# Kernel optimization log

Hardware: AMD Instinct MI355X
Metric: run time of the kernel (lower is better)

Reference implementation:

```python
import jax, jax.numpy as jnp
import numpy as np

S, B, D, H, F, E = 2048, 2, 768, 12, 3072, 8
DH = D // H
T = S * B
CAP = int(2.0 * T / E)  # capacity factor 2.0


def layer_norm(x, g, b, eps=1e-5):
    m = jnp.mean(x, axis=-1, keepdims=True)
    v = jnp.var(x, axis=-1, keepdims=True)
    return (x - m) * jax.lax.rsqrt(v + eps) * g + b


def setup_inputs() -> dict:
    key = jax.random.key(0)
    ks = jax.random.split(key, 16)
    sc = 0.02
    return {
        "src": jax.random.normal(ks[0], (S, B, D), jnp.float32),
        "in_proj_w": sc * jax.random.normal(ks[1], (3 * D, D), jnp.float32),
        "in_proj_b": sc * jax.random.normal(ks[2], (3 * D,), jnp.float32),
        "out_proj_w": sc * jax.random.normal(ks[3], (D, D), jnp.float32),
        "out_proj_b": sc * jax.random.normal(ks[4], (D,), jnp.float32),
        "norm1_g": 1.0 + sc * jax.random.normal(ks[5], (D,), jnp.float32),
        "norm1_b": sc * jax.random.normal(ks[6], (D,), jnp.float32),
        "router_w": sc * jax.random.normal(ks[7], (E, D), jnp.float32),
        "router_b": sc * jax.random.normal(ks[8], (E,), jnp.float32),
        "w1": sc * jax.random.normal(ks[9], (E, D, F), jnp.float32),
        "b1": sc * jax.random.normal(ks[10], (E, F), jnp.float32),
        "w2": sc * jax.random.normal(ks[11], (E, F, D), jnp.float32),
        "b2": sc * jax.random.normal(ks[12], (E, D), jnp.float32),
        "norm2_g": 1.0 + sc * jax.random.normal(ks[13], (D,), jnp.float32),
        "norm2_b": sc * jax.random.normal(ks[14], (D,), jnp.float32),
    }


def reference(src, in_proj_w, in_proj_b, out_proj_w, out_proj_b,
              norm1_g, norm1_b, router_w, router_b, w1, b1, w2, b2,
              norm2_g, norm2_b):
    # ---- multi-head self-attention (dropout = identity, eval mode) ----
    qkv = src @ in_proj_w.T + in_proj_b                # [S,B,3D]
    q, k, v = jnp.split(qkv, 3, axis=-1)

    def heads(t):  # [S,B,D] -> [B,H,S,DH]
        return t.reshape(S, B, H, DH).transpose(1, 2, 0, 3)

    q, k, v = heads(q), heads(k), heads(v)
    scores = jnp.einsum('bhsd,bhtd->bhst', q, k) / np.float32(np.sqrt(DH))
    attn = jax.nn.softmax(scores, axis=-1)
    ctx = jnp.einsum('bhst,bhtd->bhsd', attn, v)       # [B,H,S,DH]
    ctx = ctx.transpose(2, 0, 1, 3).reshape(S, B, D)
    attn_out = ctx @ out_proj_w.T + out_proj_b

    x = layer_norm(src + attn_out, norm1_g, norm1_b)

    # ---- Switch MoE FFN: top-1 routing, capacity-based dispatch ----
    tok = x.reshape(T, D)
    logits = tok @ router_w.T + router_b               # [T,E]
    probs = jax.nn.softmax(logits, axis=-1)
    eidx = jnp.argmax(probs, axis=-1)                  # [T]
    gate = jnp.take_along_axis(probs, eidx[:, None], axis=-1)[:, 0]
    oh = jax.nn.one_hot(eidx, E, dtype=probs.dtype)    # [T,E]
    # position of each token within its expert's queue
    pos = (jnp.cumsum(oh, axis=0) * oh).sum(-1).astype(jnp.int32) - 1

    # scatter tokens into per-expert buffers (tokens over capacity dropped)
    buf = jnp.zeros((E, CAP, D), tok.dtype).at[eidx, pos].set(tok, mode='drop')
    h = jax.nn.relu(jnp.einsum('ecd,edf->ecf', buf, w1) + b1[:, None, :])
    y = jnp.einsum('ecf,efd->ecd', h, w2) + b2[:, None, :]

    keep = pos < CAP
    out_tok = jnp.where(keep[:, None], y[eidx, jnp.minimum(pos, CAP - 1)], 0.0)
    out_tok = out_tok * gate[:, None]
    moe_out = out_tok.reshape(S, B, D)

    # load-balancing loss: E * sum_e(frac_tokens_e * mean_prob_e)
    f = oh.mean(axis=0)
    P = probs.mean(axis=0)
    lb_loss = E * jnp.sum(f * P)

    out = layer_norm(x + moe_out, norm2_g, norm2_b)
    return (out, lb_loss)
```

## Files before the change

kernel.cpp:

```cpp
#include <hip/hip_runtime.h>
#include <hip/hip_bf16.h>


#define S_   2048
#define B_   2
#define D_   768
#define H_   12
#define DH_  64
#define F_   3072
#define E_   8
#define T_   4096
#define CAP_ 1024

#define AP_  68

typedef __hip_bfloat16 bf16;
using short8  = __attribute__((ext_vector_type(8))) short;
using floatx4 = __attribute__((ext_vector_type(4))) float;

__device__ __forceinline__ float b2f(bf16 x) { return __bfloat162float(x); }
__device__ __forceinline__ bf16  f2b(float x) { return __float2bfloat16(x); }

struct SrcPair { const bf16* h; const bf16* l; };

__global__ __launch_bounds__(256) void split_kernel(
    const float* __restrict__ x, bf16* __restrict__ h, bf16* __restrict__ l,
    int n4) {
  int i = blockIdx.x * 256 + threadIdx.x;
  if (i >= n4) return;
  float4 v = ((const float4*)x)[i];
  float va[4] = {v.x, v.y, v.z, v.w};
  __attribute__((aligned(8))) bf16 hh[4], ll[4];
#pragma unroll
  for (int j = 0; j < 4; j++) {
    bf16 t = f2b(va[j]);
    hh[j] = t;
    ll[j] = f2b(va[j] - b2f(t));
  }
  *(uint2*)(h + (size_t)i * 4) = *(const uint2*)hh;
  *(uint2*)(l + (size_t)i * 4) = *(const uint2*)ll;
}

__device__ __forceinline__ void gemm_split_loop(
    SrcPair A, SrcPair W, int K,
    bf16* AsH, bf16* AsL, bf16* WsH, bf16* WsL, floatx4 (&acc)[4][4]) {
  const int tid = threadIdx.x;
  const int w = tid >> 6, lane = tid & 63;
  const int srow = lane >> 2;
  const int scol = (lane & 3) * 8;
  const int r0 = w * 32 + srow;
  const int lds0 = (w * 32 + srow) * 32 + scol;
  const int wm = (w >> 1) * 64, wn = (w & 1) * 64;
  const int fr = lane & 15, g = lane >> 4;

  size_t o0 = (size_t)r0 * K + scol;
  size_t o1 = (size_t)(r0 + 16) * K + scol;
  short8 ah0 = *(const short8*)(A.h + o0), al0 = *(const short8*)(A.l + o0);
  short8 ah1 = *(const short8*)(A.h + o1), al1 = *(const short8*)(A.l + o1);
  short8 wh0 = *(const short8*)(W.h + o0), wl0 = *(const short8*)(W.l + o0);
  short8 wh1 = *(const short8*)(W.h + o1), wl1 = *(const short8*)(W.l + o1);

  for (int kt = 0; kt < K; kt += 32) {
    o0 += 32; o1 += 32;
    __syncthreads();
    *(short8*)(AsH + lds0)       = ah0;
    *(short8*)(AsH + lds0 + 512) = ah1;
    *(short8*)(AsL + lds0)       = al0;
    *(short8*)(AsL + lds0 + 512) = al1;
    *(short8*)(WsH + lds0)       = wh0;
    *(short8*)(WsH + lds0 + 512) = wh1;
    *(short8*)(WsL + lds0)       = wl0;
    *(short8*)(WsL + lds0 + 512) = wl1;
    __syncthreads();
    if (kt + 32 < K) {
      ah0 = *(const short8*)(A.h + o0); al0 = *(const short8*)(A.l + o0);
      ah1 = *(const short8*)(A.h + o1); al1 = *(const short8*)(A.l + o1);
      wh0 = *(const short8*)(W.h + o0); wl0 = *(const short8*)(W.l + o0);
      wh1 = *(const short8*)(W.h + o1); wl1 = *(const short8*)(W.l + o1);
    }
    short8 afh[4], afl[4], bfh[4], bfl[4];
#pragma unroll
    for (int mi = 0; mi < 4; mi++) {
      int o = (wm + mi * 16 + fr) * 32 + g * 8;
      afh[mi] = *(const short8*)&AsH[o];
      afl[mi] = *(const short8*)&AsL[o];
    }
#pragma unroll
    for (int ni = 0; ni < 4; ni++) {
      int o = (wn + ni * 16 + fr) * 32 + g * 8;
      bfh[ni] = *(const short8*)&WsH[o];
      bfl[ni] = *(const short8*)&WsL[o];
    }
#pragma unroll
    for (int mi = 0; mi < 4; mi++)
#pragma unroll
      for (int ni = 0; ni < 4; ni++) {
        floatx4 z = acc[mi][ni];
        z = __builtin_amdgcn_mfma_f32_16x16x32_bf16(afh[mi], bfh[ni], z, 0, 0, 0);
        z = __builtin_amdgcn_mfma_f32_16x16x32_bf16(afh[mi], bfl[ni], z, 0, 0, 0);
        z = __builtin_amdgcn_mfma_f32_16x16x32_bf16(afl[mi], bfh[ni], z, 0, 0, 0);
        acc[mi][ni] = z;
      }
  }
}

__global__ __launch_bounds__(256) void gemm_split_pairout(
    SrcPair A, SrcPair W, const float* __restrict__ bias,
    bf16* __restrict__ Chi, bf16* __restrict__ Clo, int N, int K) {
  __shared__ __attribute__((aligned(16))) bf16 AsH[4096], AsL[4096];
  __shared__ __attribute__((aligned(16))) bf16 WsH[4096], WsL[4096];
  const int m0 = blockIdx.y * 128, n0 = blockIdx.x * 128;
  floatx4 acc[4][4];
#pragma unroll
  for (int i = 0; i < 4; i++)
#pragma unroll
    for (int j = 0; j < 4; j++) acc[i][j] = (floatx4){0.f, 0.f, 0.f, 0.f};
  SrcPair Aoff{A.h + (size_t)m0 * K, A.l + (size_t)m0 * K};
  SrcPair Woff{W.h + (size_t)n0 * K, W.l + (size_t)n0 * K};
  gemm_split_loop(Aoff, Woff, K, AsH, AsL, WsH, WsL, acc);

  const int tid = threadIdx.x, w = tid >> 6, lane = tid & 63;
  const int wm = (w >> 1) * 64, wn = (w & 1) * 64;
  const int fr = lane & 15, rg = (lane >> 4) * 4;
#pragma unroll
  for (int mi = 0; mi < 4; mi++) {
#pragma unroll
    for (int ni = 0; ni < 4; ni++) {
      int n = n0 + wn + ni * 16 + fr;
      float bv = bias[n];
#pragma unroll
      for (int r = 0; r < 4; r++) {
        int m = m0 + wm + mi * 16 + rg + r;
        float v = acc[mi][ni][r] + bv;
        bf16 hh = f2b(v);
        Chi[(size_t)m * N + n] = hh;
        Clo[(size_t)m * N + n] = f2b(v - b2f(hh));
      }
    }
  }
}

__global__ __launch_bounds__(256) void gemm_split_f32out(
    SrcPair A, SrcPair W, const float* __restrict__ bias,
    const float* __restrict__ resid, float* __restrict__ C, int N, int K) {
  __shared__ __attribute__((aligned(16))) bf16 AsH[4096], AsL[4096];
  __shared__ __attribute__((aligned(16))) bf16 WsH[4096], WsL[4096];
  const int m0 = blockIdx.y * 128, n0 = blockIdx.x * 128;
  floatx4 acc[4][4];
#pragma unroll
  for (int i = 0; i < 4; i++)
#pragma unroll
    for (int j = 0; j < 4; j++) acc[i][j] = (floatx4){0.f, 0.f, 0.f, 0.f};
  SrcPair Aoff{A.h + (size_t)m0 * K, A.l + (size_t)m0 * K};
  SrcPair Woff{W.h + (size_t)n0 * K, W.l + (size_t)n0 * K};
  gemm_split_loop(Aoff, Woff, K, AsH, AsL, WsH, WsL, acc);

  const int tid = threadIdx.x, w = tid >> 6, lane = tid & 63;
  const int wm = (w >> 1) * 64, wn = (w & 1) * 64;
  const int fr = lane & 15, rg = (lane >> 4) * 4;
#pragma unroll
  for (int mi = 0; mi < 4; mi++) {
#pragma unroll
    for (int ni = 0; ni < 4; ni++) {
      int n = n0 + wn + ni * 16 + fr;
      float bv = bias[n];
#pragma unroll
      for (int r = 0; r < 4; r++) {
        int m = m0 + wm + mi * 16 + rg + r;
        C[(size_t)m * N + n] = acc[mi][ni][r] + bv + resid[(size_t)m * N + n];
      }
    }
  }
}

__device__ __forceinline__ void gemm_tile_loop(
    const bf16* __restrict__ Ablk, const bf16* __restrict__ Wblk, int K,
    bf16* As, bf16* Ws, floatx4 (&acc)[4][4]) {
  const int tid = threadIdx.x;
  const int w = tid >> 6, lane = tid & 63;
  const int srow = lane >> 2;
  const int scol = (lane & 3) * 8;
  const bf16* Ag = Ablk + (size_t)(w * 32 + srow) * K + scol;
  const bf16* Wg = Wblk + (size_t)(w * 32 + srow) * K + scol;
  bf16* AsW = As + (w * 32 + srow) * 32 + scol;
  bf16* WsW = Ws + (w * 32 + srow) * 32 + scol;
  const int wm = (w >> 1) * 64, wn = (w & 1) * 64;
  const int fr = lane & 15, g = lane >> 4;

  short8 a0 = *(const short8*)(Ag);
  short8 a1 = *(const short8*)(Ag + 16 * (size_t)K);
  short8 w0 = *(const short8*)(Wg);
  short8 w1v = *(const short8*)(Wg + 16 * (size_t)K);

  for (int kt = 0; kt < K; kt += 32) {
    Ag += 32; Wg += 32;
    __syncthreads();
    *(short8*)(AsW)           = a0;
    *(short8*)(AsW + 16 * 32) = a1;
    *(short8*)(WsW)           = w0;
    *(short8*)(WsW + 16 * 32) = w1v;
    __syncthreads();
    if (kt + 32 < K) {
      a0 = *(const short8*)(Ag);
      a1 = *(const short8*)(Ag + 16 * (size_t)K);
      w0 = *(const short8*)(Wg);
      w1v = *(const short8*)(Wg + 16 * (size_t)K);
    }
    short8 af[4], bfg[4];
#pragma unroll
    for (int mi = 0; mi < 4; mi++)
      af[mi] = *(const short8*)&As[(wm + mi * 16 + fr) * 32 + g * 8];
#pragma unroll
    for (int ni = 0; ni < 4; ni++)
      bfg[ni] = *(const short8*)&Ws[(wn + ni * 16 + fr) * 32 + g * 8];
#pragma unroll
    for (int mi = 0; mi < 4; mi++)
#pragma unroll
      for (int ni = 0; ni < 4; ni++)
        acc[mi][ni] = __builtin_amdgcn_mfma_f32_16x16x32_bf16(
            af[mi], bfg[ni], acc[mi][ni], 0, 0, 0);
  }
}

__global__ __launch_bounds__(256) void moe1_kernel(
    const bf16* __restrict__ xe, const bf16* __restrict__ w1t,
    const float* __restrict__ b1, bf16* __restrict__ h,
    const int* __restrict__ counts) {
  const int e = blockIdx.y >> 3, lt = blockIdx.y & 7;
  int kept = counts[e]; if (kept > CAP_) kept = CAP_;
  if (lt * 128 >= kept) return;
  __shared__ __attribute__((aligned(16))) bf16 As[4096];
  __shared__ __attribute__((aligned(16))) bf16 Ws[4096];
  const int n0 = blockIdx.x * 128;
  floatx4 acc[4][4];
#pragma unroll
  for (int i = 0; i < 4; i++)
#pragma unroll
    for (int j = 0; j < 4; j++) acc[i][j] = (floatx4){0.f, 0.f, 0.f, 0.f};
  gemm_tile_loop(xe + (size_t)(e * CAP_ + lt * 128) * D_,
                 w1t + (size_t)e * F_ * D_ + (size_t)n0 * D_, D_, As, Ws, acc);

  const int tid = threadIdx.x, w = tid >> 6, lane = tid & 63;
  const int wm = (w >> 1) * 64, wn = (w & 1) * 64;
  const int fr = lane & 15, rg = (lane >> 4) * 4;
#pragma unroll
  for (int mi = 0; mi < 4; mi++) {
#pragma unroll
    for (int ni = 0; ni < 4; ni++) {
      int n = n0 + wn + ni * 16 + fr;
      float bv = b1[e * F_ + n];
#pragma unroll
      for (int r = 0; r < 4; r++) {
        int mrow = lt * 128 + wm + mi * 16 + rg + r;
        h[(size_t)(e * CAP_ + mrow) * F_ + n] =
            f2b(fmaxf(acc[mi][ni][r] + bv, 0.f));
      }
    }
  }
}

__global__ __launch_bounds__(256) void moe2_kernel(
    const bf16* __restrict__ h, const bf16* __restrict__ w2t,
    const float* __restrict__ bias2, const int* __restrict__ stok,
    const float* __restrict__ sgate, const int* __restrict__ counts,
    bf16* __restrict__ moe) {
  const int e = blockIdx.y >> 3, lt = blockIdx.y & 7;
  int kept = counts[e]; if (kept > CAP_) kept = CAP_;
  if (lt * 128 >= kept) return;
  __shared__ __attribute__((aligned(16))) bf16 As[4096];
  __shared__ __attribute__((aligned(16))) bf16 Ws[4096];
  const int n0 = blockIdx.x * 128;
  floatx4 acc[4][4];
#pragma unroll
  for (int i = 0; i < 4; i++)
#pragma unroll
    for (int j = 0; j < 4; j++) acc[i][j] = (floatx4){0.f, 0.f, 0.f, 0.f};
  gemm_tile_loop(h + (size_t)(e * CAP_ + lt * 128) * F_,
                 w2t + (size_t)e * D_ * F_ + (size_t)n0 * F_, F_, As, Ws, acc);

  const int tid = threadIdx.x, w = tid >> 6, lane = tid & 63;
  const int wm = (w >> 1) * 64, wn = (w & 1) * 64;
  const int fr = lane & 15, rg = (lane >> 4) * 4;
#pragma unroll
  for (int mi = 0; mi < 4; mi++) {
#pragma unroll
    for (int r = 0; r < 4; r++) {
      int mrow = lt * 128 + wm + mi * 16 + rg + r;
      int slot = e * CAP_ + mrow;
      int t = stok[slot];
      if (t < 0) continue;
      float gt = sgate[slot];
#pragma unroll
      for (int ni = 0; ni < 4; ni++) {
        int n = n0 + wn + ni * 16 + fr;
        moe[(size_t)t * D_ + n] = f2b((acc[mi][ni][r] + bias2[e * D_ + n]) * gt);
      }
    }
  }
}

__global__ __launch_bounds__(256) void vtrans2_kernel(
    const bf16* __restrict__ qh, const bf16* __restrict__ ql,
    bf16* __restrict__ vth, bf16* __restrict__ vtl) {
  __shared__ bf16 th[64][65], tl[64][65];
  const int tid = threadIdx.x;
  const int bh = blockIdx.y, b = bh / H_, hh = bh % H_;
  const int s0 = blockIdx.x * 64;
#pragma unroll
  for (int i = 0; i < 2; i++) {
    int rr = i * 32 + tid / 8, cc = (tid % 8) * 8;
    size_t off = (size_t)((s0 + rr) * B_ + b) * (3 * D_) + 2 * D_ + hh * DH_ + cc;
    short8 vh = *(const short8*)(qh + off);
    short8 vl = *(const short8*)(ql + off);
    const bf16* ph = (const bf16*)&vh;
    const bf16* pl = (const bf16*)&vl;
#pragma unroll
    for (int j = 0; j < 8; j++) { th[rr][cc + j] = ph[j]; tl[rr][cc + j] = pl[j]; }
  }
  __syncthreads();
#pragma unroll
  for (int i = 0; i < 2; i++) {
    int cc = i * 32 + tid / 8, rr = (tid % 8) * 8;
    __attribute__((aligned(16))) bf16 a[8], c[8];
#pragma unroll
    for (int j = 0; j < 8; j++) { a[j] = th[rr + j][cc]; c[j] = tl[rr + j][cc]; }
    size_t off = ((size_t)bh * DH_ + cc) * S_ + s0 + rr;
    *(short8*)(vth + off) = *(const short8*)a;
    *(short8*)(vtl + off) = *(const short8*)c;
  }
}

__global__ __launch_bounds__(256) void attn_kernel(
    const bf16* __restrict__ qh, const bf16* __restrict__ ql,
    const bf16* __restrict__ vth, const bf16* __restrict__ vtl,
    bf16* __restrict__ ch, bf16* __restrict__ cl) {
  __shared__ __attribute__((aligned(16))) bf16 KsH[64 * AP_], KsL[64 * AP_];
  __shared__ __attribute__((aligned(16))) bf16 VsH[64 * AP_], VsL[64 * AP_];
  __shared__ __attribute__((aligned(16))) bf16 PsH[4][16 * AP_], PsL[4][16 * AP_];
  const int tid = threadIdx.x, w = tid >> 6, lane = tid & 63;
  const int bh = blockIdx.y, b = bh / H_, hh = bh % H_;
  const int q0 = blockIdx.x * 64;
  const int fr = lane & 15, g = lane >> 4;

  const int qs = q0 + w * 16 + fr;
  const size_t qoff = (size_t)(qs * B_ + b) * (3 * D_) + hh * DH_;
  const short8 qf0h = *(const short8*)(qh + qoff + g * 8);
  const short8 qf1h = *(const short8*)(qh + qoff + 32 + g * 8);
  const short8 qf0l = *(const short8*)(ql + qoff + g * 8);
  const short8 qf1l = *(const short8*)(ql + qoff + 32 + g * 8);

  float mi_[4], li_[4], alpha[4];
  floatx4 o[4];
#pragma unroll
  for (int r = 0; r < 4; r++) { mi_[r] = -1e30f; li_[r] = 0.f; }
#pragma unroll
  for (int nt = 0; nt < 4; nt++) o[nt] = (floatx4){0.f, 0.f, 0.f, 0.f};

  const int str = tid >> 2;
  const int st16 = (tid & 3) * 16;

  size_t koff = (size_t)(str * B_ + b) * (3 * D_) + D_ + hh * DH_ + st16;
  size_t voff = ((size_t)bh * DH_ + str) * S_ + st16;
  short8 pk0h = *(const short8*)(qh + koff);
  short8 pk1h = *(const short8*)(qh + koff + 8);
  short8 pk0l = *(const short8*)(ql + koff);
  short8 pk1l = *(const short8*)(ql + koff + 8);
  short8 pv0h = *(const short8*)(vth + voff);
  short8 pv1h = *(const short8*)(vth + voff + 8);
  short8 pv0l = *(const short8*)(vtl + voff);
  short8 pv1l = *(const short8*)(vtl + voff + 8);

  for (int kb = 0; kb < S_ / 64; kb++) {
    __syncthreads();
    *(short8*)&KsH[str * AP_ + st16]     = pk0h;
    *(short8*)&KsH[str * AP_ + st16 + 8] = pk1h;
    *(short8*)&KsL[str * AP_ + st16]     = pk0l;
    *(short8*)&KsL[str * AP_ + st16 + 8] = pk1l;
    *(short8*)&VsH[str * AP_ + st16]     = pv0h;
    *(short8*)&VsH[str * AP_ + st16 + 8] = pv1h;
    *(short8*)&VsL[str * AP_ + st16]     = pv0l;
    *(short8*)&VsL[str * AP_ + st16 + 8] = pv1l;
    __syncthreads();

    if (kb + 1 < S_ / 64) {
      size_t k2 = koff + (size_t)64 * B_ * (3 * D_) * (kb + 1 - kb);
      koff += (size_t)64 * B_ * (3 * D_);
      voff += 64;
      (void)k2;
      pk0h = *(const short8*)(qh + koff);
      pk1h = *(const short8*)(qh + koff + 8);
      pk0l = *(const short8*)(ql + koff);
      pk1l = *(const short8*)(ql + koff + 8);
      pv0h = *(const short8*)(vth + voff);
      pv1h = *(const short8*)(vth + voff + 8);
      pv0l = *(const short8*)(vtl + voff);
      pv1l = *(const short8*)(vtl + voff + 8);
    }

    floatx4 sc[4];
#pragma unroll
    for (int nt = 0; nt < 4; nt++) {
      int krow = nt * 16 + fr;
      short8 k0h = *(const short8*)&KsH[krow * AP_ + g * 8];
      short8 k1h = *(const short8*)&KsH[krow * AP_ + 32 + g * 8];
      short8 k0l = *(const short8*)&KsL[krow * AP_ + g * 8];
      short8 k1l = *(const short8*)&KsL[krow * AP_ + 32 + g * 8];
      floatx4 z = (floatx4){0.f, 0.f, 0.f, 0.f};
      z = __builtin_amdgcn_mfma_f32_16x16x32_bf16(qf0h, k0h, z, 0, 0, 0);
      z = __builtin_amdgcn_mfma_f32_16x16x32_bf16(qf1h, k1h, z, 0, 0, 0);
      z = __builtin_amdgcn_mfma_f32_16x16x32_bf16(qf0h, k0l, z, 0, 0, 0);
      z = __builtin_amdgcn_mfma_f32_16x16x32_bf16(qf1h, k1l, z, 0, 0, 0);
      z = __builtin_amdgcn_mfma_f32_16x16x32_bf16(qf0l, k0h, z, 0, 0, 0);
      z = __builtin_amdgcn_mfma_f32_16x16x32_bf16(qf1l, k1h, z, 0, 0, 0);
      sc[nt] = z;
    }
#pragma unroll
    for (int nt = 0; nt < 4; nt++)
#pragma unroll
      for (int r = 0; r < 4; r++) sc[nt][r] *= 0.125f;

#pragma unroll
    for (int r = 0; r < 4; r++) {
      float mx = fmaxf(fmaxf(sc[0][r], sc[1][r]), fmaxf(sc[2][r], sc[3][r]));
#pragma unroll
      for (int d = 1; d < 16; d <<= 1) mx = fmaxf(mx, __shfl_xor(mx, d));
      float mn = fmaxf(mi_[r], mx);
      alpha[r] = __expf(mi_[r] - mn);
      float rs = 0.f;
#pragma unroll
      for (int nt = 0; nt < 4; nt++) {
        float p = __expf(sc[nt][r] - mn);
        sc[nt][r] = p; rs += p;
      }
#pragma unroll
      for (int d = 1; d < 16; d <<= 1) rs += __shfl_xor(rs, d);
      li_[r] = li_[r] * alpha[r] + rs;
      mi_[r] = mn;
    }
#pragma unroll
    for (int nt = 0; nt < 4; nt++)
#pragma unroll
      for (int r = 0; r < 4; r++) o[nt][r] *= alpha[r];

    bf16* PwH = &PsH[w][0];
    bf16* PwL = &PsL[w][0];
#pragma unroll
    for (int nt = 0; nt < 4; nt++)
#pragma unroll
      for (int r = 0; r < 4; r++) {
        float p = sc[nt][r];
        bf16 hh2 = f2b(p);
        PwH[((g << 2) + r) * AP_ + nt * 16 + fr] = hh2;
        PwL[((g << 2) + r) * AP_ + nt * 16 + fr] = f2b(p - b2f(hh2));
      }
    asm volatile("s_waitcnt lgkmcnt(0)" ::: "memory");

    short8 p0h = *(const short8*)&PwH[fr * AP_ + g * 8];
    short8 p1h = *(const short8*)&PwH[fr * AP_ + 32 + g * 8];
    short8 p0l = *(const short8*)&PwL[fr * AP_ + g * 8];
    short8 p1l = *(const short8*)&PwL[fr * AP_ + 32 + g * 8];
#pragma unroll
    for (int nt = 0; nt < 4; nt++) {
      int dh = nt * 16 + fr;
      short8 v0h = *(const short8*)&VsH[dh * AP_ + g * 8];
      short8 v1h = *(const short8*)&VsH[dh * AP_ + 32 + g * 8];
      short8 v0l = *(const short8*)&VsL[dh * AP_ + g * 8];
      short8 v1l = *(const short8*)&VsL[dh * AP_ + 32 + g * 8];
      floatx4 z = o[nt];
      z = __builtin_amdgcn_mfma_f32_16x16x32_bf16(p0h, v0h, z, 0, 0, 0);
      z = __builtin_amdgcn_mfma_f32_16x16x32_bf16(p1h, v1h, z, 0, 0, 0);
      z = __builtin_amdgcn_mfma_f32_16x16x32_bf16(p0h, v0l, z, 0, 0, 0);
      z = __builtin_amdgcn_mfma_f32_16x16x32_bf16(p1h, v1l, z, 0, 0, 0);
      z = __builtin_amdgcn_mfma_f32_16x16x32_bf16(p0l, v0h, z, 0, 0, 0);
      z = __builtin_amdgcn_mfma_f32_16x16x32_bf16(p1l, v1h, z, 0, 0, 0);
      o[nt] = z;
    }
  }

#pragma unroll
  for (int nt = 0; nt < 4; nt++) {
#pragma unroll
    for (int r = 0; r < 4; r++) {
      int qrow = q0 + w * 16 + (g << 2) + r;
      float li = fmaxf(li_[r], 1e-20f);
      float v = o[nt][r] / li;
      size_t off = (size_t)(qrow * B_ + b) * D_ + hh * DH_ + nt * 16 + fr;
      bf16 hh2 = f2b(v);
      ch[off] = hh2;
      cl[off] = f2b(v - b2f(hh2));
    }
  }
}

__global__ __launch_bounds__(256) void transpose_kernel(
    const float* __restrict__ src, bf16* __restrict__ dst, int R, int C) {
  __shared__ bf16 tile[64][65];
  const int tid = threadIdx.x;
  const size_t boff = (size_t)blockIdx.z * R * C;
  const int c0 = blockIdx.x * 64, r0 = blockIdx.y * 64;
#pragma unroll
  for (int i = 0; i < 2; i++) {
    int rr = i * 32 + tid / 8, cc = (tid % 8) * 8;
    const float* sp = &src[boff + (size_t)(r0 + rr) * C + c0 + cc];
    float4 v0 = *(const float4*)sp;
    float4 v1 = *(const float4*)(sp + 4);
    tile[rr][cc + 0] = f2b(v0.x); tile[rr][cc + 1] = f2b(v0.y);
    tile[rr][cc + 2] = f2b(v0.z); tile[rr][cc + 3] = f2b(v0.w);
    tile[rr][cc + 4] = f2b(v1.x); tile[rr][cc + 5] = f2b(v1.y);
    tile[rr][cc + 6] = f2b(v1.z); tile[rr][cc + 7] = f2b(v1.w);
  }
  __syncthreads();
#pragma unroll
  for (int i = 0; i < 2; i++) {
    int cc = i * 32 + tid / 8, rr = (tid % 8) * 8;
    __attribute__((aligned(16))) bf16 tmp[8];
#pragma unroll
    for (int j = 0; j < 8; j++) tmp[j] = tile[rr + j][cc];
    *(short8*)&dst[boff + (size_t)(c0 + cc) * R + r0 + rr] =
        *(const short8*)tmp;
  }
}

__global__ __launch_bounds__(256) void ln_kernel(
    const float* __restrict__ x, const bf16* __restrict__ add,
    const float* __restrict__ gam, const float* __restrict__ bet,
    float* __restrict__ out) {
  const int row = blockIdx.x, tid = threadIdx.x;
  float v[3], s = 0.f, sq = 0.f;
#pragma unroll
  for (int j = 0; j < 3; j++) {
    int c = tid + j * 256;
    float t = x[(size_t)row * D_ + c];
    if (add) t += b2f(add[(size_t)row * D_ + c]);
    v[j] = t; s += t; sq += t * t;
  }
#pragma unroll
  for (int d = 1; d < 64; d <<= 1) { s += __shfl_xor(s, d); sq += __shfl_xor(sq, d); }
  __shared__ float ss[4], ssq[4];
  const int w = tid >> 6, lane = tid & 63;
  if (lane == 0) { ss[w] = s; ssq[w] = sq; }
  __syncthreads();
  s = ss[0] + ss[1] + ss[2] + ss[3];
  sq = ssq[0] + ssq[1] + ssq[2] + ssq[3];
  float mean = s * (1.f / D_);
  float var = fmaxf(sq * (1.f / D_) - mean * mean, 0.f);
  float rstd = rsqrtf(var + 1e-5f);
#pragma unroll
  for (int j = 0; j < 3; j++) {
    int c = tid + j * 256;
    out[(size_t)row * D_ + c] = (v[j] - mean) * rstd * gam[c] + bet[c];
  }
}

__global__ __launch_bounds__(256) void router_kernel(
    const float* __restrict__ x, const float* __restrict__ rw,
    const float* __restrict__ rb, float* __restrict__ probs,
    int* __restrict__ eidx, float* __restrict__ gate) {
  const int tid = threadIdx.x, w = tid >> 6, lane = tid & 63;
  const int t = blockIdx.x * 4 + w;
  float acc[E_];
#pragma unroll
  for (int e = 0; e < E_; e++) acc[e] = 0.f;
  for (int j = 0; j < D_ / 64; j++) {
    int c = lane + j * 64;
    float xv = x[(size_t)t * D_ + c];
#pragma unroll
    for (int e = 0; e < E_; e++) acc[e] += xv * rw[e * D_ + c];
  }
#pragma unroll
  for (int e = 0; e < E_; e++)
#pragma unroll
    for (int d = 1; d < 64; d <<= 1) acc[e] += __shfl_xor(acc[e], d);
  if (lane == 0) {
    float lg[E_], p[E_], mx = -1e30f;
#pragma unroll
    for (int e = 0; e < E_; e++) { lg[e] = acc[e] + rb[e]; mx = fmaxf(mx, lg[e]); }
    float sum = 0.f;
#pragma unroll
    for (int e = 0; e < E_; e++) { p[e] = __expf(lg[e] - mx); sum += p[e]; }
    float inv = 1.f / sum;
    int am = 0; float bm = lg[0];
#pragma unroll
    for (int e = 1; e < E_; e++) if (lg[e] > bm) { bm = lg[e]; am = e; }
#pragma unroll
    for (int e = 0; e < E_; e++) probs[t * E_ + e] = p[e] * inv;
    eidx[t] = am;
    gate[t] = p[am] * inv;
  }
}

__global__ __launch_bounds__(512) void router_pos_kernel(
    const int* __restrict__ eidx, const float* __restrict__ probs,
    const float* __restrict__ gate, int* __restrict__ stok,
    float* __restrict__ sgate, int* __restrict__ counts,
    float* __restrict__ lb_out) {
  const int tid = threadIdx.x, e = tid >> 6, lane = tid & 63;
  int base = 0; float sump = 0.f;
  for (int c = 0; c < T_ / 64; c++) {
    int t = c * 64 + lane;
    int ei = eidx[t];
    sump += probs[t * E_ + e];
    bool m = (ei == e);
    unsigned long long mask = __ballot(m);
    if (m) {
      int p = base + (int)__popcll(mask & ((1ull << lane) - 1ull));
      if (p < CAP_) {
        stok[e * CAP_ + p] = t;
        sgate[e * CAP_ + p] = gate[t];
      }
    }
    base += (int)__popcll(mask);
  }
#pragma unroll
  for (int d = 1; d < 64; d <<= 1) sump += __shfl_xor(sump, d);
  __shared__ float sP[E_];
  __shared__ int sC[E_];
  if (lane == 0) { counts[e] = base; sC[e] = base; sP[e] = sump; }
  __syncthreads();
  if (tid == 0) {
    float lb = 0.f;
    for (int i = 0; i < E_; i++) lb += (float)sC[i] * sP[i];
    lb *= (float)E_ / ((float)T_ * (float)T_);
    lb_out[0] = lb;
  }
}

__global__ __launch_bounds__(256) void gather_kernel(
    const float* __restrict__ x, const int* __restrict__ stok,
    bf16* __restrict__ xe) {
  int idx = blockIdx.x * 256 + threadIdx.x;
  int slot = idx / (D_ / 4), r = idx % (D_ / 4);
  int t = stok[slot];
  bf16 o0, o1, o2, o3;
  if (t >= 0) {
    float4 v = *(const float4*)(x + (size_t)t * D_ + r * 4);
    o0 = f2b(v.x); o1 = f2b(v.y); o2 = f2b(v.z); o3 = f2b(v.w);
  } else {
    o0 = o1 = o2 = o3 = f2b(0.f);
  }
  bf16* dst = xe + (size_t)slot * D_ + r * 4;
  dst[0] = o0; dst[1] = o1; dst[2] = o2; dst[3] = o3;
}

extern "C" void kernel_launch(void* const* d_in, const int* in_sizes, int n_in,
                              void* d_out, int out_size, void* d_ws,
                              size_t ws_size, hipStream_t stream) {
  const float* src   = (const float*)d_in[0];
  const float* in_w  = (const float*)d_in[1];
  const float* in_b  = (const float*)d_in[2];
  const float* out_w = (const float*)d_in[3];
  const float* out_b = (const float*)d_in[4];
  const float* n1g   = (const float*)d_in[5];
  const float* n1b   = (const float*)d_in[6];
  const float* rw    = (const float*)d_in[7];
  const float* rb    = (const float*)d_in[8];
  const float* w1    = (const float*)d_in[9];
  const float* b1    = (const float*)d_in[10];
  const float* w2    = (const float*)d_in[11];
  const float* b2p   = (const float*)d_in[12];
  const float* n2g   = (const float*)d_in[13];
  const float* n2b   = (const float*)d_in[14];
  float* out = (float*)d_out;

  char* ws = (char*)d_ws;
  bf16*  qkv_h  = (bf16*)(ws + 0);
  bf16*  qkv_l  = (bf16*)(ws + 18874368);
  bf16*  w1t    = (bf16*)(ws + 0);
  bf16*  w2t    = (bf16*)(ws + 0);
  bf16*  ctx_h  = (bf16*)(ws + 37748736);
  bf16*  ctx_l  = (bf16*)(ws + 44040192);
  bf16*  xe     = (bf16*)(ws + 37748736);
  bf16*  moe    = (bf16*)(ws + 37748736);
  float* xln    = (float*)(ws + 50331648);
  bf16*  vt_h   = (bf16*)(ws + 62914560);
  bf16*  vt_l   = (bf16*)(ws + 69206016);
  bf16*  hbuf   = (bf16*)(ws + 62914560);
  bf16*  src_h  = (bf16*)(ws + 75497472);
  bf16*  src_l  = (bf16*)(ws + 81788928);
  bf16*  inw_h  = (bf16*)(ws + 88080384);
  bf16*  inw_l  = (bf16*)(ws + 91619328);
  bf16*  outw_h = (bf16*)(ws + 95158272);
  bf16*  outw_l = (bf16*)(ws + 96337920);
  float* probs  = (float*)(ws + 113246208);
  int*   eidx   = (int*)(ws + 113377280);
  float* gate   = (float*)(ws + 113393664);
  int*   counts = (int*)(ws + 113410048);
  int*   stok   = (int*)(ws + 113410304);
  float* sgate  = (float*)(ws + 113443072);

  (void)in_sizes; (void)n_in; (void)out_size; (void)ws_size;

  hipMemsetAsync(stok, 0xFF, E_ * CAP_ * sizeof(int), stream);

  split_kernel<<<(T_ * D_ / 4) / 256, 256, 0, stream>>>(src, src_h, src_l,
                                                        T_ * D_ / 4);
  split_kernel<<<(3 * D_ * D_ / 4) / 256, 256, 0, stream>>>(
      in_w, inw_h, inw_l, 3 * D_ * D_ / 4);
  split_kernel<<<(D_ * D_ / 4) / 256, 256, 0, stream>>>(out_w, outw_h, outw_l,
                                                        D_ * D_ / 4);

  gemm_split_pairout<<<dim3(3 * D_ / 128, T_ / 128), 256, 0, stream>>>(
      SrcPair{src_h, src_l}, SrcPair{inw_h, inw_l}, in_b, qkv_h, qkv_l,
      3 * D_, D_);
  vtrans2_kernel<<<dim3(S_ / 64, B_ * H_), 256, 0, stream>>>(
      qkv_h, qkv_l, vt_h, vt_l);
  attn_kernel<<<dim3(S_ / 64, B_ * H_), 256, 0, stream>>>(
      qkv_h, qkv_l, vt_h, vt_l, ctx_h, ctx_l);
  gemm_split_f32out<<<dim3(D_ / 128, T_ / 128), 256, 0, stream>>>(
      SrcPair{ctx_h, ctx_l}, SrcPair{outw_h, outw_l}, out_b, src, xln, D_, D_);
  ln_kernel<<<T_, 256, 0, stream>>>(xln, nullptr, n1g, n1b, xln);
  router_kernel<<<T_ / 4, 256, 0, stream>>>(xln, rw, rb, probs, eidx, gate);
  router_pos_kernel<<<1, 512, 0, stream>>>(eidx, probs, gate, stok, sgate,
                                           counts, out + (size_t)T_ * D_);
  gather_kernel<<<(E_ * CAP_ * (D_ / 4)) / 256, 256, 0, stream>>>(xln, stok, xe);
  transpose_kernel<<<dim3(F_ / 64, D_ / 64, E_), 256, 0, stream>>>(w1, w1t, D_, F_);
  moe1_kernel<<<dim3(F_ / 128, E_ * (CAP_ / 128)), 256, 0, stream>>>(
      xe, w1t, b1, hbuf, counts);
  hipMemsetAsync(moe, 0, (size_t)T_ * D_ * sizeof(bf16), stream);
  transpose_kernel<<<dim3(D_ / 64, F_ / 64, E_), 256, 0, stream>>>(w2, w2t, F_, D_);
  moe2_kernel<<<dim3(D_ / 128, E_ * (CAP_ / 128)), 256, 0, stream>>>(
      hbuf, w2t, b2p, stok, sgate, counts, moe);
  ln_kernel<<<T_, 256, 0, stream>>>(xln, moe, n2g, n2b, out);
}
```

Before: 703.5 us.

## Load GEMM tiles directly to LDS and alias attention P buffer onto K

The GEMM inner loops now issue global_load_lds instructions that copy global memory straight into shared memory, replacing register prefetch followed by LDS stores, and add a trailing barrier per K step. This gives up the register-level prefetch overlap, so loads are no longer issued a step ahead of the MFMAs. Separately, the attention kernel reuses the K tile's shared memory for the per-wave P buffers, with an extra barrier, and raises launch bounds to request 4 blocks per CU. The aim is to cut LDS footprint and raise occupancy, at the cost of more synchronisation.

```diff
diff --git a/kernel.cpp b/kernel.cpp
--- a/kernel.cpp
+++ b/kernel.cpp
@@ -21,6 +21,12 @@
 __device__ __forceinline__ float b2f(bf16 x) { return __bfloat162float(x); }
 __device__ __forceinline__ bf16  f2b(float x) { return __float2bfloat16(x); }
 
+__device__ __forceinline__ void gld_lds16(const bf16* g, bf16* l) {
+  __builtin_amdgcn_global_load_lds(
+      (const __attribute__((address_space(1))) void*)g,
+      (__attribute__((address_space(3))) void*)l, 16, 0, 0);
+}
+
 struct SrcPair { const bf16* h; const bf16* l; };
 
 __global__ __launch_bounds__(256) void split_kernel(
@@ -48,36 +54,24 @@
   const int w = tid >> 6, lane = tid & 63;
   const int srow = lane >> 2;
   const int scol = (lane & 3) * 8;
-  const int r0 = w * 32 + srow;
-  const int lds0 = (w * 32 + srow) * 32 + scol;
+  const bf16* Ah = A.h + (size_t)(w * 32 + srow) * K + scol;
+  const bf16* Al = A.l + (size_t)(w * 32 + srow) * K + scol;
+  const bf16* Wh = W.h + (size_t)(w * 32 + srow) * K + scol;
+  const bf16* Wl = W.l + (size_t)(w * 32 + srow) * K + scol;
+  bf16* AsHb = AsH + w * 1024;
+  bf16* AsLb = AsL + w * 1024;
+  bf16* WsHb = WsH + w * 1024;
+  bf16* WsLb = WsL + w * 1024;
   const int wm = (w >> 1) * 64, wn = (w & 1) * 64;
   const int fr = lane & 15, g = lane >> 4;
 
-  size_t o0 = (size_t)r0 * K + scol;
-  size_t o1 = (size_t)(r0 + 16) * K + scol;
-  short8 ah0 = *(const short8*)(A.h + o0), al0 = *(const short8*)(A.l + o0);
-  short8 ah1 = *(const short8*)(A.h + o1), al1 = *(const short8*)(A.l + o1);
-  short8 wh0 = *(const short8*)(W.h + o0), wl0 = *(const short8*)(W.l + o0);
-  short8 wh1 = *(const short8*)(W.h + o1), wl1 = *(const short8*)(W.l + o1);
-
   for (int kt = 0; kt < K; kt += 32) {
-    o0 += 32; o1 += 32;
+    gld_lds16(Ah, AsHb); gld_lds16(Ah + 16 * (size_t)K, AsHb + 512);
+    gld_lds16(Al, AsLb); gld_lds16(Al + 16 * (size_t)K, AsLb + 512);
+    gld_lds16(Wh, WsHb); gld_lds16(Wh + 16 * (size_t)K, WsHb + 512);
+    gld_lds16(Wl, WsLb); gld_lds16(Wl + 16 * (size_t)K, WsLb + 512);
+    Ah += 32; Al += 32; Wh += 32; Wl += 32;
     __syncthreads();
-    *(short8*)(AsH + lds0)       = ah0;
-    *(short8*)(AsH + lds0 + 512) = ah1;
-    *(short8*)(AsL + lds0)       = al0;
-    *(short8*)(AsL + lds0 + 512) = al1;
-    *(short8*)(WsH + lds0)       = wh0;
-    *(short8*)(WsH + lds0 + 512) = wh1;
-    *(short8*)(WsL + lds0)       = wl0;
-    *(short8*)(WsL + lds0 + 512) = wl1;
-    __syncthreads();
-    if (kt + 32 < K) {
-      ah0 = *(const short8*)(A.h + o0); al0 = *(const short8*)(A.l + o0);
-      ah1 = *(const short8*)(A.h + o1); al1 = *(const short8*)(A.l + o1);
-      wh0 = *(const short8*)(W.h + o0); wl0 = *(const short8*)(W.l + o0);
-      wh1 = *(const short8*)(W.h + o1); wl1 = *(const short8*)(W.l + o1);
-    }
     short8 afh[4], afl[4], bfh[4], bfl[4];
 #pragma unroll
     for (int mi = 0; mi < 4; mi++) {
@@ -101,6 +95,7 @@
         z = __builtin_amdgcn_mfma_f32_16x16x32_bf16(afl[mi], bfh[ni], z, 0, 0, 0);
         acc[mi][ni] = z;
       }
+    __syncthreads();
   }
 }
 
@@ -182,30 +177,16 @@
   const int scol = (lane & 3) * 8;
   const bf16* Ag = Ablk + (size_t)(w * 32 + srow) * K + scol;
   const bf16* Wg = Wblk + (size_t)(w * 32 + srow) * K + scol;
-  bf16* AsW = As + (w * 32 + srow) * 32 + scol;
-  bf16* WsW = Ws + (w * 32 + srow) * 32 + scol;
+  bf16* Asb = As + w * 1024;
+  bf16* Wsb = Ws + w * 1024;
   const int wm = (w >> 1) * 64, wn = (w & 1) * 64;
   const int fr = lane & 15, g = lane >> 4;
 
-  short8 a0 = *(const short8*)(Ag);
-  short8 a1 = *(const short8*)(Ag + 16 * (size_t)K);
-  short8 w0 = *(const short8*)(Wg);
-  short8 w1v = *(const short8*)(Wg + 16 * (size_t)K);
-
   for (int kt = 0; kt < K; kt += 32) {
+    gld_lds16(Ag, Asb); gld_lds16(Ag + 16 * (size_t)K, Asb + 512);
+    gld_lds16(Wg, Wsb); gld_lds16(Wg + 16 * (size_t)K, Wsb + 512);
     Ag += 32; Wg += 32;
     __syncthreads();
-    *(short8*)(AsW)           = a0;
-    *(short8*)(AsW + 16 * 32) = a1;
-    *(short8*)(WsW)           = w0;
-    *(short8*)(WsW + 16 * 32) = w1v;
-    __syncthreads();
-    if (kt + 32 < K) {
-      a0 = *(const short8*)(Ag);
-      a1 = *(const short8*)(Ag + 16 * (size_t)K);
-      w0 = *(const short8*)(Wg);
-      w1v = *(const short8*)(Wg + 16 * (size_t)K);
-    }
     short8 af[4], bfg[4];
 #pragma unroll
     for (int mi = 0; mi < 4; mi++)
@@ -219,6 +200,7 @@
       for (int ni = 0; ni < 4; ni++)
         acc[mi][ni] = __builtin_amdgcn_mfma_f32_16x16x32_bf16(
             af[mi], bfg[ni], acc[mi][ni], 0, 0, 0);
+    __syncthreads();
   }
 }
 
@@ -330,17 +312,20 @@
   }
 }
 
-__global__ __launch_bounds__(256) void attn_kernel(
+__global__ __launch_bounds__(256, 4) void attn_kernel(
     const bf16* __restrict__ qh, const bf16* __restrict__ ql,
     const bf16* __restrict__ vth, const bf16* __restrict__ vtl,
     bf16* __restrict__ ch, bf16* __restrict__ cl) {
-  __shared__ __attribute__((aligned(16))) bf16 KsH[64 * AP_], KsL[64 * AP_];
+  __shared__ __attribute__((aligned(16))) bf16 KP[2 * 64 * AP_];
   __shared__ __attribute__((aligned(16))) bf16 VsH[64 * AP_], VsL[64 * AP_];
-  __shared__ __attribute__((aligned(16))) bf16 PsH[4][16 * AP_], PsL[4][16 * AP_];
   const int tid = threadIdx.x, w = tid >> 6, lane = tid & 63;
   const int bh = blockIdx.y, b = bh / H_, hh = bh % H_;
   const int q0 = blockIdx.x * 64;
   const int fr = lane & 15, g = lane >> 4;
+  bf16* KsH = KP;
+  bf16* KsL = KP + 64 * AP_;
+  bf16* PwH = KP + w * (16 * AP_);
+  bf16* PwL = KP + 64 * AP_ + w * (16 * AP_);
 
   const int qs = q0 + w * 16 + fr;
   const size_t qoff = (size_t)(qs * B_ + b) * (3 * D_) + hh * DH_;
@@ -383,10 +368,8 @@
     __syncthreads();
 
     if (kb + 1 < S_ / 64) {
-      size_t k2 = koff + (size_t)64 * B_ * (3 * D_) * (kb + 1 - kb);
       koff += (size_t)64 * B_ * (3 * D_);
       voff += 64;
-      (void)k2;
       pk0h = *(const short8*)(qh + koff);
       pk1h = *(const short8*)(qh + koff + 8);
       pk0l = *(const short8*)(ql + koff);
@@ -442,8 +425,8 @@
 #pragma unroll
       for (int r = 0; r < 4; r++) o[nt][r] *= alpha[r];
 
-    bf16* PwH = &PsH[w][0];
-    bf16* PwL = &PsL[w][0];
+    __syncthreads();
+
 #pragma unroll
     for (int nt = 0; nt < 4; nt++)
 #pragma unroll
```

New measurement: 881.6 us. 1.25x slower.
